# Kernel tuning notes

Measured on AMD Instinct MI355X. Metric: run time of the kernel, lower is better.

The kernel has to match this reference:

```python
import jax, jax.numpy as jnp
import numpy as np
from jax import lax

VOCAB = 100000
E = 300          # embedding_dim
H = 256          # hidden_dim
B = 1024         # batch (also LSTM time length after view(1, B, 3E+3))
LENS = (200, 400, 600)
D_IN = 3 * E + 3
EPS = 1e-8


def setup_inputs() -> dict:
    key = jax.random.key(0)
    ks = jax.random.split(key, 16)
    s = 0.05
    inp = {
        "x": jax.random.randint(ks[0], (B, LENS[2]), 0, VOCAB, dtype=jnp.int64)
        if jax.config.jax_enable_x64 else
        jax.random.randint(ks[0], (B, LENS[2]), 0, VOCAB).astype(jnp.int32),
        "h0": jnp.zeros((2, 1, H), jnp.float32),
        "c0": jnp.zeros((2, 1, H), jnp.float32),
        "emb": jax.random.normal(ks[1], (VOCAB, E), jnp.float32),
        "w_ih0": jax.random.normal(ks[2], (4 * H, D_IN), jnp.float32) * s,
        "w_hh0": jax.random.normal(ks[3], (4 * H, H), jnp.float32) * s,
        "b_ih0": jax.random.normal(ks[4], (4 * H,), jnp.float32) * s,
        "b_hh0": jax.random.normal(ks[5], (4 * H,), jnp.float32) * s,
        "w_ih1": jax.random.normal(ks[6], (4 * H, H), jnp.float32) * s,
        "w_hh1": jax.random.normal(ks[7], (4 * H, H), jnp.float32) * s,
        "b_ih1": jax.random.normal(ks[8], (4 * H,), jnp.float32) * s,
        "b_hh1": jax.random.normal(ks[9], (4 * H,), jnp.float32) * s,
        "fc_w": jax.random.normal(ks[10], (1, H), jnp.float32) * s,
        "fc_b": jax.random.normal(ks[11], (1,), jnp.float32) * s,
    }
    return inp


def _cos(a, b):
    # F.cosine_similarity semantics with eps clamp on each norm
    na = jnp.maximum(jnp.linalg.norm(a, axis=-1), EPS)
    nb = jnp.maximum(jnp.linalg.norm(b, axis=-1), EPS)
    return jnp.sum(a * b, axis=-1) / (na * nb)


def _conv(x, emb):
    # vectorized version of the per-sample python loop:
    # segment SUM over all tokens divided by count of NONZERO tokens (faithful).
    e = emb[x]  # [B, 600, E]  (the big memory-bound gather)
    def seg(a, b):
        s = e[:, a:b].sum(axis=1)                              # [B, E]
        cnt = (x[:, a:b] != 0).sum(axis=1).astype(e.dtype)     # [B]
        return s / cnt[:, None]
    st = seg(0, LENS[0])
    su = seg(LENS[0], LENS[1])
    ju = seg(LENS[1], LENS[2])
    ret = jnp.concatenate(
        [st, _cos(st, su)[:, None],
         su, _cos(su, ju)[:, None],
         ju, _cos(st, ju)[:, None]], axis=1)                   # [B, 3E+3]
    return ret


def _lstm_layer(xs, h, c, w_ih, w_hh, b_ih, b_hh):
    # xs: [T, Din]; batch size is 1, so carry is vectors. PyTorch gate order i,f,g,o.
    def step(carry, xt):
        h, c = carry
        g = xt @ w_ih.T + b_ih + h @ w_hh.T + b_hh   # [4H]
        i, f, gg, o = jnp.split(g, 4)
        i, f, o = jax.nn.sigmoid(i), jax.nn.sigmoid(f), jax.nn.sigmoid(o)
        c = f * c + i * jnp.tanh(gg)
        h = o * jnp.tanh(c)
        return (h, c), h
    (hn, cn), ys = lax.scan(step, (h, c), xs)
    return ys, hn, cn


def reference(x, h0, c0, emb, w_ih0, w_hh0, b_ih0, b_hh0,
              w_ih1, w_hh1, b_ih1, b_hh1, fc_w, fc_b):
    xs = _conv(x, emb)                                  # [B, 3E+3] (seq for LSTM)
    ys1, h1, c1 = _lstm_layer(xs, h0[0, 0], c0[0, 0], w_ih0, w_hh0, b_ih0, b_hh0)
    ys2, h2, c2 = _lstm_layer(ys1, h0[1, 0], c0[1, 0], w_ih1, w_hh1, b_ih1, b_hh1)
    # dropout layers are identity in eval mode
    out = jax.nn.sigmoid(ys2 @ fc_w.T + fc_b)           # [B, 1]
    sig_out = out[:, -1]                                # [B]
    hn = jnp.stack([h1, h2])[:, None, :]                # [2,1,H]
    cn = jnp.stack([c1, c2])[:, None, :]
    return sig_out, hn, cn
```

## Files before the change

### kernel.cpp

```cpp
#include <hip/hip_runtime.h>
#include <math.h>

#define NB    1024
#define SEQ   600
#define EDIM  300
#define HDIM  256
#define DIN   903
#define GDIM  1024

#define SENT  0xFFFFFFFFu

__device__ __forceinline__ float fsig(float x) {
    return __builtin_amdgcn_rcpf(1.f + __builtin_amdgcn_exp2f(x * -1.44269504f));
}
__device__ __forceinline__ float ftanh(float x) {
    return 1.f - 2.f * __builtin_amdgcn_rcpf(1.f + __builtin_amdgcn_exp2f(x * 2.88539008f));
}

__device__ __forceinline__ float row16_sum(float x) {
    x += __int_as_float(__builtin_amdgcn_update_dpp(0, __float_as_int(x), 0x128, 0xf, 0xf, true));
    x += __int_as_float(__builtin_amdgcn_update_dpp(0, __float_as_int(x), 0x124, 0xf, 0xf, true));
    x += __int_as_float(__builtin_amdgcn_update_dpp(0, __float_as_int(x), 0x122, 0xf, 0xf, true));
    x += __int_as_float(__builtin_amdgcn_update_dpp(0, __float_as_int(x), 0x121, 0xf, 0xf, true));
    return x;
}

__device__ __forceinline__ void lds_barrier() {
    asm volatile("s_waitcnt lgkmcnt(0)" ::: "memory");
    __builtin_amdgcn_s_barrier();
}

__device__ __forceinline__ float poll_f(const float* p) {
    const unsigned* up = (const unsigned*)p;
    unsigned u; int gd = 0;
    do { u = __hip_atomic_load(up, __ATOMIC_RELAXED, __HIP_MEMORY_SCOPE_AGENT); }
    while (u == SENT && ++gd < (1 << 24));
    return __uint_as_float(u);
}
__device__ __forceinline__ void st_f(float* p, float v) {
    __hip_atomic_store(p, v, __ATOMIC_RELAXED, __HIP_MEMORY_SCOPE_AGENT);
}

__global__ __launch_bounds__(256) void conv_kernel(const int* __restrict__ x,
                                                   const float* __restrict__ emb,
                                                   float* __restrict__ X) {
    const int row = blockIdx.x;
    const int tid = threadIdx.x;
    const int* xr = x + (size_t)row * SEQ;

    __shared__ float seg[3][EDIM];
    __shared__ float scnt[3];
    __shared__ float reds[6];
    __shared__ float coss[3];

    if (tid < 6) reds[tid] = 0.f;
    if (tid < 3) scnt[tid] = 0.f;
    __syncthreads();

    {
        int c0 = 0, c1 = 0, c2 = 0;
        for (int t = tid; t < 200; t += 256) {
            c0 += (xr[t]       != 0);
            c1 += (xr[200 + t] != 0);
            c2 += (xr[400 + t] != 0);
        }
        float f0 = (float)c0, f1 = (float)c1, f2 = (float)c2;
        #pragma unroll
        for (int m = 1; m < 64; m <<= 1) {
            f0 += __shfl_xor(f0, m);
            f1 += __shfl_xor(f1, m);
            f2 += __shfl_xor(f2, m);
        }
        if ((tid & 63) == 0) {
            atomicAdd(&scnt[0], f0);
            atomicAdd(&scnt[1], f1);
            atomicAdd(&scnt[2], f2);
        }
    }
    __syncthreads();

    const float inv0 = 1.f / scnt[0], inv1 = 1.f / scnt[1], inv2 = 1.f / scnt[2];

    for (int d = tid; d < EDIM; d += 256) {
        float a0 = 0.f, a1 = 0.f, a2 = 0.f;
        for (int t = 0; t < 200; t++) {
            a0 += emb[(size_t)xr[t]       * EDIM + d];
            a1 += emb[(size_t)xr[200 + t] * EDIM + d];
            a2 += emb[(size_t)xr[400 + t] * EDIM + d];
        }
        seg[0][d] = a0 * inv0;
        seg[1][d] = a1 * inv1;
        seg[2][d] = a2 * inv2;
    }
    __syncthreads();

    {
        float p0 = 0, p1 = 0, p2 = 0, p3 = 0, p4 = 0, p5 = 0;
        for (int d = tid; d < EDIM; d += 256) {
            float a = seg[0][d], b = seg[1][d], c = seg[2][d];
            p0 += a * a; p1 += b * b; p2 += c * c;
            p3 += a * b; p4 += b * c; p5 += a * c;
        }
        #pragma unroll
        for (int m = 1; m < 64; m <<= 1) {
            p0 += __shfl_xor(p0, m); p1 += __shfl_xor(p1, m);
            p2 += __shfl_xor(p2, m); p3 += __shfl_xor(p3, m);
            p4 += __shfl_xor(p4, m); p5 += __shfl_xor(p5, m);
        }
        if ((tid & 63) == 0) {
            atomicAdd(&reds[0], p0); atomicAdd(&reds[1], p1);
            atomicAdd(&reds[2], p2); atomicAdd(&reds[3], p3);
            atomicAdd(&reds[4], p4); atomicAdd(&reds[5], p5);
        }
    }
    __syncthreads();
    if (tid == 0) {
        float nt = fmaxf(sqrtf(reds[0]), 1e-8f);
        float nu = fmaxf(sqrtf(reds[1]), 1e-8f);
        float nj = fmaxf(sqrtf(reds[2]), 1e-8f);
        coss[0] = reds[3] / (nt * nu);
        coss[1] = reds[4] / (nu * nj);
        coss[2] = reds[5] / (nt * nj);
    }
    __syncthreads();

    float* Xr = X + (size_t)row * DIN;
    for (int col = tid; col < DIN; col += 256) {
        float v;
        if      (col < 300)  v = seg[0][col];
        else if (col == 300) v = coss[0];
        else if (col < 601)  v = seg[1][col - 301];
        else if (col == 601) v = coss[1];
        else if (col < 902)  v = seg[2][col - 602];
        else                 v = coss[2];
        Xr[col] = v;
    }
}

__global__ __launch_bounds__(256) void gemm_bias(const float* __restrict__ A,
                                                 const float* __restrict__ Bm,
                                                 const float* __restrict__ bias1,
                                                 const float* __restrict__ bias2,
                                                 float* __restrict__ C, int K) {
    __shared__ float As[16][68];
    __shared__ float Bs[16][68];
    const int tid = threadIdx.x;
    const int tx = tid & 15, ty = tid >> 4;
    const int m0 = blockIdx.y * 64, n0 = blockIdx.x * 64;

    float acc[4][4] = {};
    for (int k0 = 0; k0 < K; k0 += 16) {
        #pragma unroll
        for (int i = 0; i < 4; i++) {
            int e  = tid + i * 256;
            int rr = e >> 4, kk = e & 15;
            int k  = k0 + kk;
            As[kk][rr] = (k < K) ? A[(size_t)(m0 + rr) * K + k] : 0.f;
            Bs[kk][rr] = (k < K) ? Bm[(size_t)(n0 + rr) * K + k] : 0.f;
        }
        __syncthreads();
        #pragma unroll
        for (int kk = 0; kk < 16; kk++) {
            float a[4], b[4];
            #pragma unroll
            for (int i = 0; i < 4; i++) { a[i] = As[kk][ty * 4 + i]; b[i] = Bs[kk][tx * 4 + i]; }
            #pragma unroll
            for (int i = 0; i < 4; i++)
                #pragma unroll
                for (int j = 0; j < 4; j++)
                    acc[i][j] += a[i] * b[j];
        }
        __syncthreads();
    }
    #pragma unroll
    for (int i = 0; i < 4; i++) {
        int m = m0 + ty * 4 + i;
        #pragma unroll
        for (int j = 0; j < 4; j++) {
            int n = n0 + tx * 4 + j;
            C[(size_t)m * GDIM + n] = acc[i][j] + bias1[n] + bias2[n];
        }
    }
}

__global__ __launch_bounds__(512) void lstm_fused(
    const float* __restrict__ G1,
    const float* __restrict__ Whh0,
    const float* __restrict__ Wih1,
    const float* __restrict__ Whh1,
    const float* __restrict__ b_ih1,
    const float* __restrict__ b_hh1,
    const float* __restrict__ h0,
    const float* __restrict__ c0,
    float* mailA, float* mailX, float* mailB, float* mailP,
    float* ys2, float* out)
{
    const int tid = threadIdx.x;
    const int bid = blockIdx.x;
    const int l   = tid & 63;
    const int v   = tid >> 6;
    const int k   = l >> 4;
    const int q   = l & 15;

    __shared__ __align__(16) float hb[2][16][20];

    if (bid < 16) {
        const int  L = bid >> 3;
        const int  m = bid & 7;
        const int  e = m * 32 + 4 * v + k;
        const int  eloc = e & 31;
        const float* Wh = L ? Whh1 : Whh0;
        float* mailH = L ? mailB : mailA;

        float4 w[4][4];
        #pragma unroll
        for (int g = 0; g < 4; g++)
            #pragma unroll
            for (int j = 0; j < 4; j++)
                w[g][j] = *(const float4*)&Wh[(size_t)(g * 256 + e) * HDIM + q * 16 + j * 4];

        float c = c0[L * HDIM + e];

        for (int t = 0; t < NB; t++) {
            const int nb = t & 1;

            float gq = 0.f;
            unsigned gu = 0;
            const unsigned* gp = nullptr;
            if (q < 4) {
                if (L == 0) {
                    gq = G1[(size_t)t * GDIM + q * 256 + e];
                } else {
                    gp = (const unsigned*)(mailP + ((size_t)m * NB + t) * 128 + q * 32 + eloc);
                    gu = __hip_atomic_load(gp, __ATOMIC_RELAXED, __HIP_MEMORY_SCOPE_AGENT);
                }
            }

            if (tid < HDIM) {
                if (t == 0) {
                    hb[0][tid >> 4][tid & 15] = h0[L * HDIM + tid];
                } else if ((tid >> 5) != m) {
                    hb[nb][tid >> 4][tid & 15] =
                        poll_f(mailH + ((size_t)m * NB + (t - 1)) * HDIM + tid);
                }
            }
            lds_barrier();

            float a0 = 0.f, a1 = 0.f, a2 = 0.f, a3 = 0.f;
            #pragma unroll
            for (int j = 0; j < 4; j++) {
                float4 hv = *(const float4*)&hb[nb][q][j * 4];
                float4 w0 = w[0][j], w1 = w[1][j], w2 = w[2][j], w3 = w[3][j];
                a0 += hv.x * w0.x + hv.y * w0.y + hv.z * w0.z + hv.w * w0.w;
                a1 += hv.x * w1.x + hv.y * w1.y + hv.z * w1.z + hv.w * w1.w;
                a2 += hv.x * w2.x + hv.y * w2.y + hv.z * w2.z + hv.w * w2.w;
                a3 += hv.x * w3.x + hv.y * w3.y + hv.z * w3.z + hv.w * w3.w;
            }

            if (q < 4) {
                if (L == 1) {
                    int gd = 0;
                    while (gu == SENT && ++gd < (1 << 24))
                        gu = __hip_atomic_load(gp, __ATOMIC_RELAXED, __HIP_MEMORY_SCOPE_AGENT);
                    gq = __uint_as_float(gu);
                }
                if      (q == 0) a0 += gq;
                else if (q == 1) a1 += gq;
                else if (q == 2) a2 += gq;
                else             a3 += gq;
            }

            a0 = row16_sum(a0); a1 = row16_sum(a1);
            a2 = row16_sum(a2); a3 = row16_sum(a3);

            float ig = fsig(a0), fg = fsig(a1), og = fsig(a3);
            c = fg * c + ig * ftanh(a2);
            float h = og * ftanh(c);

            if (q == 4) hb[nb ^ 1][e >> 4][e & 15] = h;
            if (q == 0) {
                #pragma unroll
                for (int r = 0; r < 4; r++)
                    if (r != m) st_f(mailH + ((size_t)r * NB + t) * HDIM + e, h);
            }
            if (q == 1) {
                #pragma unroll
                for (int r = 4; r < 8; r++)
                    if (r != m) st_f(mailH + ((size_t)r * NB + t) * HDIM + e, h);
            }
            if (L == 0) {
                if (q == 2) {
                    st_f(mailX + ((size_t)0 * NB + t) * HDIM + e, h);
                    st_f(mailX + ((size_t)1 * NB + t) * HDIM + e, h);
                }
                if (q == 3) {
                    st_f(mailX + ((size_t)2 * NB + t) * HDIM + e, h);
                    st_f(mailX + ((size_t)3 * NB + t) * HDIM + e, h);
                }
            } else {
                if (q == 2) ys2[(size_t)t * HDIM + e] = h;
            }
            if (t == NB - 1 && q == 5) {
                out[1024 + L * HDIM + e] = h;
                out[1536 + L * HDIM + e] = c;
            }
        }
    } else {
        const int n = bid - 16;
        const int e = n * 32 + 4 * v + k;
        const int eloc = e & 31;
        const float* xsrc = mailX + (size_t)(n >> 1) * NB * HDIM;

        float4 w[4][4];
        #pragma unroll
        for (int g = 0; g < 4; g++)
            #pragma unroll
            for (int j = 0; j < 4; j++)
                w[g][j] = *(const float4*)&Wih1[(size_t)(g * 256 + e) * HDIM + q * 16 + j * 4];

        float bsum = 0.f;
        if (q < 4) bsum = b_ih1[q * 256 + e] + b_hh1[q * 256 + e];

        for (int t = 0; t < NB; t++) {
            const int nb = t & 1;
            if (tid < HDIM)
                hb[nb][tid >> 4][tid & 15] = poll_f(xsrc + (size_t)t * HDIM + tid);
            lds_barrier();

            float a0 = 0.f, a1 = 0.f, a2 = 0.f, a3 = 0.f;
            #pragma unroll
            for (int j = 0; j < 4; j++) {
                float4 hv = *(const float4*)&hb[nb][q][j * 4];
                float4 w0 = w[0][j], w1 = w[1][j], w2 = w[2][j], w3 = w[3][j];
                a0 += hv.x * w0.x + hv.y * w0.y + hv.z * w0.z + hv.w * w0.w;
                a1 += hv.x * w1.x + hv.y * w1.y + hv.z * w1.z + hv.w * w1.w;
                a2 += hv.x * w2.x + hv.y * w2.y + hv.z * w2.z + hv.w * w2.w;
                a3 += hv.x * w3.x + hv.y * w3.y + hv.z * w3.z + hv.w * w3.w;
            }
            a0 = row16_sum(a0); a1 = row16_sum(a1);
            a2 = row16_sum(a2); a3 = row16_sum(a3);

            if (q < 4) {
                float pv = (q == 0 ? a0 : q == 1 ? a1 : q == 2 ? a2 : a3) + bsum;
                st_f(mailP + ((size_t)n * NB + t) * 128 + q * 32 + eloc, pv);
            }
        }
    }
}

__global__ __launch_bounds__(256) void fc_kernel(const float* __restrict__ ys2,
                                                 const float* __restrict__ fc_w,
                                                 const float* __restrict__ fc_b,
                                                 float* __restrict__ out) {
    const int row  = blockIdx.x * 4 + (threadIdx.x >> 6);
    const int lane = threadIdx.x & 63;
    float4 y = ((const float4*)(ys2 + (size_t)row * HDIM))[lane];
    float4 wv = ((const float4*)fc_w)[lane];
    float d = y.x * wv.x + y.y * wv.y + y.z * wv.z + y.w * wv.w;
    #pragma unroll
    for (int m = 1; m < 64; m <<= 1) d += __shfl_xor(d, m);
    if (lane == 0) out[row] = 1.f / (1.f + expf(-(d + fc_b[0])));
}

extern "C" void kernel_launch(void* const* d_in, const int* in_sizes, int n_in,
                              void* d_out, int out_size, void* d_ws, size_t ws_size,
                              hipStream_t stream) {
    const int*   x     = (const int*)  d_in[0];
    const float* h0    = (const float*)d_in[1];
    const float* c0    = (const float*)d_in[2];
    const float* emb   = (const float*)d_in[3];
    const float* w_ih0 = (const float*)d_in[4];
    const float* w_hh0 = (const float*)d_in[5];
    const float* b_ih0 = (const float*)d_in[6];
    const float* b_hh0 = (const float*)d_in[7];
    const float* w_ih1 = (const float*)d_in[8];
    const float* w_hh1 = (const float*)d_in[9];
    const float* b_ih1 = (const float*)d_in[10];
    const float* b_hh1 = (const float*)d_in[11];
    const float* fc_w  = (const float*)d_in[12];
    const float* fc_b  = (const float*)d_in[13];
    float* out = (float*)d_out;

    float* mail  = (float*)d_ws;
    float* mailA = mail;
    float* mailX = mailA + (size_t)8 * NB * HDIM;
    float* mailB = mailX + (size_t)4 * NB * HDIM;
    float* mailP = mailB + (size_t)8 * NB * HDIM;
    float* G1    = mailP + (size_t)8 * NB * 128;
    float* ys2   = G1    + (size_t)NB * GDIM;
    float* X     = mail;

    conv_kernel<<<NB, 256, 0, stream>>>(x, emb, X);

    gemm_bias<<<dim3(16, 16), 256, 0, stream>>>(X, w_ih0, b_ih0, b_hh0, G1, DIN);

    hipMemsetAsync(mail, 0xFF, (size_t)(8 + 4 + 8) * NB * HDIM * sizeof(float)
                               + (size_t)8 * NB * 128 * sizeof(float), stream);

    lstm_fused<<<24, 512, 0, stream>>>(G1, w_hh0, w_ih1, w_hh1, b_ih1, b_hh1,
                                       h0, c0, mailA, mailX, mailB, mailP,
                                       ys2, out);

    fc_kernel<<<NB / 4, 256, 0, stream>>>(ys2, fc_w, fc_b, out);
}
```

Baseline: 2.205 ms.

## Co-locate recurrent LSTM blocks on one XCD and poll mailboxes with fast volatile loads

The fused LSTM kernel now launches 192 blocks. Each block reads its XCC id and claims a slot through atomic counters, so the 16 recurrent blocks can be placed on the first XCD that collects 16 blocks, while 8 others take the input-projection role and the rest exit. On the co-located path, the h-vector mailboxes are polled with plain volatile loads, which are meant to hit the shared L2 instead of going through agent-scope atomics. If a poll times out, the block falls back to agent-scope polling, and writers store both ways. Mailbox fan-out is cut to four shared copies, the memset is moved and a control area is added; the extra blocks, the dual stores and the reliance on the hardware register add overhead and coherence risk.

```diff
diff --git a/kernel.cpp b/kernel.cpp
--- a/kernel.cpp
+++ b/kernel.cpp
@@ -30,15 +30,19 @@
     __builtin_amdgcn_s_barrier();
 }
 
-__device__ __forceinline__ float poll_f(const float* p) {
+__device__ __forceinline__ float poll_agent(const float* p) {
     const unsigned* up = (const unsigned*)p;
     unsigned u; int gd = 0;
     do { u = __hip_atomic_load(up, __ATOMIC_RELAXED, __HIP_MEMORY_SCOPE_AGENT); }
-    while (u == SENT && ++gd < (1 << 24));
+    while (u == SENT && ++gd < (1 << 22));
     return __uint_as_float(u);
 }
-__device__ __forceinline__ void st_f(float* p, float v) {
+__device__ __forceinline__ void st_agent(float* p, float v) {
     __hip_atomic_store(p, v, __ATOMIC_RELAXED, __HIP_MEMORY_SCOPE_AGENT);
+}
+__device__ __forceinline__ void st_dual(float* p, float v) {
+    __hip_atomic_store(p, v, __ATOMIC_RELAXED, __HIP_MEMORY_SCOPE_AGENT);
+    *(volatile float*)p = v;
 }
 
 __global__ __launch_bounds__(256) void conv_kernel(const int* __restrict__ x,
@@ -192,25 +196,55 @@
     const float* __restrict__ b_hh1,
     const float* __restrict__ h0,
     const float* __restrict__ c0,
-    float* mailA, float* mailX, float* mailB, float* mailP,
+    unsigned* ctrl,
+    float* mailA, float* mailB, float* mailX, float* mailP,
     float* ys2, float* out)
 {
     const int tid = threadIdx.x;
-    const int bid = blockIdx.x;
     const int l   = tid & 63;
     const int v   = tid >> 6;
     const int k   = l >> 4;
     const int q   = l & 15;
 
     __shared__ __align__(16) float hb[2][16][20];
-
-    if (bid < 16) {
-        const int  L = bid >> 3;
-        const int  m = bid & 7;
+    __shared__ int sh_role;
+    __shared__ int sh_fast;
+
+    if (tid == 0) {
+        unsigned xcd;
+        asm volatile("s_getreg_b32 %0, hwreg(HW_REG_XCC_ID)" : "=s"(xcd));
+        xcd &= 7u;
+        unsigned slot = atomicAdd(&ctrl[xcd], 1u);
+        if (slot == 15u) atomicCAS(&ctrl[8], 0u, xcd + 1u);
+        unsigned ch = 0;
+        for (int gd = 0; gd < (1 << 14); gd++) {
+            ch = __hip_atomic_load(&ctrl[8], __ATOMIC_RELAXED, __HIP_MEMORY_SCOPE_AGENT);
+            if (ch != 0u) break;
+        }
+        int role = -1, fast = 0;
+        if (ch != 0u && xcd == ch - 1u && slot < 16u) {
+            role = (int)slot; fast = 1;
+        } else if (ch != 0u) {
+            unsigned xs = atomicAdd(&ctrl[9], 1u);
+            if (xs < 8u) role = 16 + (int)xs;
+        } else {
+            if (blockIdx.x < 24) role = blockIdx.x;
+        }
+        sh_role = role;
+        sh_fast = fast;
+    }
+    __syncthreads();
+    const int role = sh_role;
+    if (role < 0) return;
+
+    if (role < 16) {
+        const int  L = role >> 3;
+        const int  m = role & 7;
         const int  e = m * 32 + 4 * v + k;
         const int  eloc = e & 31;
         const float* Wh = L ? Whh1 : Whh0;
         float* mailH = L ? mailB : mailA;
+        const float* mailIn = mailH + (size_t)(m >> 1) * NB * HDIM;
 
         float4 w[4][4];
         #pragma unroll
@@ -240,8 +274,18 @@
                 if (t == 0) {
                     hb[0][tid >> 4][tid & 15] = h0[L * HDIM + tid];
                 } else if ((tid >> 5) != m) {
-                    hb[nb][tid >> 4][tid & 15] =
-                        poll_f(mailH + ((size_t)m * NB + (t - 1)) * HDIM + tid);
+                    const float* p = mailIn + (size_t)(t - 1) * HDIM + tid;
+                    float val;
+                    if (sh_fast) {
+                        const volatile unsigned* vp = (const volatile unsigned*)p;
+                        unsigned u = *vp; int gd = 0;
+                        while (u == SENT && ++gd < 8192) u = *vp;
+                        if (u == SENT) { sh_fast = 0; val = poll_agent(p); }
+                        else val = __uint_as_float(u);
+                    } else {
+                        val = poll_agent(p);
+                    }
+                    hb[nb][tid >> 4][tid & 15] = val;
                 }
             }
             lds_barrier();
@@ -260,7 +304,7 @@
             if (q < 4) {
                 if (L == 1) {
                     int gd = 0;
-                    while (gu == SENT && ++gd < (1 << 24))
+                    while (gu == SENT && ++gd < (1 << 22))
                         gu = __hip_atomic_load(gp, __ATOMIC_RELAXED, __HIP_MEMORY_SCOPE_AGENT);
                     gq = __uint_as_float(gu);
                 }
@@ -279,24 +323,16 @@
 
             if (q == 4) hb[nb ^ 1][e >> 4][e & 15] = h;
             if (q == 0) {
-                #pragma unroll
-                for (int r = 0; r < 4; r++)
-                    if (r != m) st_f(mailH + ((size_t)r * NB + t) * HDIM + e, h);
+                st_dual(mailH + ((size_t)0 * NB + t) * HDIM + e, h);
+                st_dual(mailH + ((size_t)1 * NB + t) * HDIM + e, h);
             }
             if (q == 1) {
-                #pragma unroll
-                for (int r = 4; r < 8; r++)
-                    if (r != m) st_f(mailH + ((size_t)r * NB + t) * HDIM + e, h);
+                st_dual(mailH + ((size_t)2 * NB + t) * HDIM + e, h);
+                st_dual(mailH + ((size_t)3 * NB + t) * HDIM + e, h);
             }
             if (L == 0) {
-                if (q == 2) {
-                    st_f(mailX + ((size_t)0 * NB + t) * HDIM + e, h);
-                    st_f(mailX + ((size_t)1 * NB + t) * HDIM + e, h);
-                }
-                if (q == 3) {
-                    st_f(mailX + ((size_t)2 * NB + t) * HDIM + e, h);
-                    st_f(mailX + ((size_t)3 * NB + t) * HDIM + e, h);
-                }
+                if (q == 2) st_agent(mailX + ((size_t)0 * NB + t) * HDIM + e, h);
+                if (q == 3) st_agent(mailX + ((size_t)1 * NB + t) * HDIM + e, h);
             } else {
                 if (q == 2) ys2[(size_t)t * HDIM + e] = h;
             }
@@ -306,10 +342,10 @@
             }
         }
     } else {
-        const int n = bid - 16;
+        const int n = role - 16;
         const int e = n * 32 + 4 * v + k;
         const int eloc = e & 31;
-        const float* xsrc = mailX + (size_t)(n >> 1) * NB * HDIM;
+        const float* xsrc = mailX + (size_t)(n >> 2) * NB * HDIM;
 
         float4 w[4][4];
         #pragma unroll
@@ -324,7 +360,7 @@
         for (int t = 0; t < NB; t++) {
             const int nb = t & 1;
             if (tid < HDIM)
-                hb[nb][tid >> 4][tid & 15] = poll_f(xsrc + (size_t)t * HDIM + tid);
+                hb[nb][tid >> 4][tid & 15] = poll_agent(xsrc + (size_t)t * HDIM + tid);
             lds_barrier();
 
             float a0 = 0.f, a1 = 0.f, a2 = 0.f, a3 = 0.f;
@@ -342,7 +378,7 @@
 
             if (q < 4) {
                 float pv = (q == 0 ? a0 : q == 1 ? a1 : q == 2 ? a2 : a3) + bsum;
-                st_f(mailP + ((size_t)n * NB + t) * 128 + q * 32 + eloc, pv);
+                st_agent(mailP + ((size_t)n * NB + t) * 128 + q * 32 + eloc, pv);
             }
         }
     }
@@ -381,25 +417,27 @@
     const float* fc_b  = (const float*)d_in[13];
     float* out = (float*)d_out;
 
-    float* mail  = (float*)d_ws;
-    float* mailA = mail;
-    float* mailX = mailA + (size_t)8 * NB * HDIM;
-    float* mailB = mailX + (size_t)4 * NB * HDIM;
-    float* mailP = mailB + (size_t)8 * NB * HDIM;
+    float*    base  = (float*)d_ws;
+    unsigned* ctrl  = (unsigned*)d_ws;
+    float* mailA = base  + 256;
+    float* mailB = mailA + (size_t)4 * NB * HDIM;
+    float* mailX = mailB + (size_t)4 * NB * HDIM;
+    float* mailP = mailX + (size_t)2 * NB * HDIM;
     float* G1    = mailP + (size_t)8 * NB * 128;
     float* ys2   = G1    + (size_t)NB * GDIM;
-    float* X     = mail;
+    float* X     = ys2   + (size_t)NB * HDIM;
+
+    hipMemsetAsync(ctrl, 0, 1024, stream);
+    hipMemsetAsync(mailA, 0xFF, ((size_t)(4 + 4 + 2) * NB * HDIM
+                                 + (size_t)8 * NB * 128) * sizeof(float), stream);
 
     conv_kernel<<<NB, 256, 0, stream>>>(x, emb, X);
 
     gemm_bias<<<dim3(16, 16), 256, 0, stream>>>(X, w_ih0, b_ih0, b_hh0, G1, DIN);
 
-    hipMemsetAsync(mail, 0xFF, (size_t)(8 + 4 + 8) * NB * HDIM * sizeof(float)
-                               + (size_t)8 * NB * 128 * sizeof(float), stream);
-
-    lstm_fused<<<24, 512, 0, stream>>>(G1, w_hh0, w_ih1, w_hh1, b_ih1, b_hh1,
-                                       h0, c0, mailA, mailX, mailB, mailP,
-                                       ys2, out);
+    lstm_fused<<<192, 512, 0, stream>>>(G1, w_hh0, w_ih1, w_hh1, b_ih1, b_hh1,
+                                        h0, c0, ctrl,
+                                        mailA, mailB, mailX, mailP, ys2, out);
 
     fc_kernel<<<NB / 4, 256, 0, stream>>>(ys2, fc_w, fc_b, out);
 }
```

Measured after the change: 3.357 ms. 52.2% more time.
